# Performance work log

Measured on AMD Instinct MI355X. Metric: run time of the kernel, lower is better.

Reference implementation:

```python
import jax, jax.numpy as jnp
import numpy as np

B = 4096          # batch_size
D_EMB = 16        # per-side embedding dim (embed_to_from width = 2*D_EMB)
D_HIGH = 784      # flattened high-dim feature size
NSR = 5           # negative_sample_rate
A = 1.576943      # UMAP _a
B_PARAM = 0.8950608  # UMAP _b
REPULSION = 1.0
EPS = 1e-4
GLOBAL_LOSS = 0.5
TOTAL_STEPS = 1000
BATCH_COUNT = 500  # fixed step for deterministic alpha/beta
WARMUP = int(0.05 * TOTAL_STEPS)


def _safe_sqrt(sq):
    # sqrt with zero (not NaN) gradient at 0, matching zero-distance pairs
    safe = jnp.where(sq > 0, sq, 1.0)
    return jnp.where(sq > 0, jnp.sqrt(safe), 0.0)


def _pairwise_dist(x):
    # ||x_i - x_j|| via gram trick; avoids materializing [N,N,D]
    sq = jnp.sum(x * x, axis=1)                      # [N]
    gram = x @ x.T                                   # [N,N]
    d2 = sq[:, None] + sq[None, :] - 2.0 * gram
    return _safe_sqrt(jnp.maximum(d2, 0.0))


def _umap_ce_loss(embed_to_from, perm):
    e_to, e_from = jnp.split(embed_to_from, 2, axis=1)   # [B, D_EMB] each
    neg_to = jnp.repeat(e_to, NSR, axis=0)               # [B*NSR, D_EMB]
    repeat_neg = jnp.repeat(e_from, NSR, axis=0)
    neg_from = repeat_neg[perm]                          # shuffled negatives
    d_pos = _safe_sqrt(jnp.sum((e_to - e_from) ** 2, axis=1))
    d_neg = _safe_sqrt(jnp.sum((neg_to - neg_from) ** 2, axis=1))
    dist = jnp.concatenate([d_pos, d_neg], axis=0)       # [B*(1+NSR)]
    p_dist = 1.0 / (1.0 + A * dist ** (2.0 * B_PARAM))
    p_graph = jnp.concatenate([jnp.ones(B, p_dist.dtype), jnp.zeros(B * NSR, p_dist.dtype)])
    attraction = -p_graph * jnp.log(jnp.clip(p_dist, EPS, 1.0))
    repellant = -(1.0 - p_graph) * jnp.log(jnp.clip(1.0 - p_dist, EPS, 1.0)) * REPULSION
    return jnp.mean(attraction + repellant)


def _global_feature_loss(embed_to_from, to_x):
    e_to = embed_to_from[:, :D_EMB]
    to_x = to_x.reshape(to_x.shape[0], -1)
    high_dis = _pairwise_dist(to_x)     # [N,N]
    low_dis = _pairwise_dist(e_to)      # [N,N]
    # row-wise pearson correlation between high_dis and low_dis
    h = high_dis - jnp.mean(high_dis, axis=1, keepdims=True)
    l = low_dis - jnp.mean(low_dis, axis=1, keepdims=True)
    num = jnp.sum(h * l, axis=1)
    den = jnp.sqrt(jnp.sum(h * h, axis=1)) * jnp.sqrt(jnp.sum(l * l, axis=1))
    corr = jnp.mean(num / den)
    return -corr


def _alpha_beta():
    if BATCH_COUNT >= WARMUP:
        if BATCH_COUNT <= 0.9 * TOTAL_STEPS:
            beta = max(0.0, GLOBAL_LOSS * (1 - BATCH_COUNT / (TOTAL_STEPS - WARMUP * 4)) ** 2)
        else:
            beta = 0.0
        alpha = max(0.0, 1 - beta)
    else:
        alpha = 0.0
        beta = GLOBAL_LOSS
    return alpha, beta


def setup_inputs() -> dict:
    key = jax.random.key(0)
    k1, k2, k3 = jax.random.split(key, 3)
    embed_to_from = jax.random.normal(k1, (B, 2 * D_EMB), dtype=jnp.float32)
    placeholder = jax.random.normal(k2, (B, D_HIGH), dtype=jnp.float32)
    perm = jax.random.permutation(k3, B * NSR).astype(jnp.int32)
    return {"embed_to_from": embed_to_from, "placeholder": placeholder, "perm": perm}


def reference(embed_to_from, placeholder, perm):
    loss = _umap_ce_loss(embed_to_from, perm)
    loss_g = _global_feature_loss(embed_to_from, placeholder)
    alpha, beta = _alpha_beta()
    return alpha * loss + beta * loss_g
```

## Files before the change

kernel.cpp:

```cpp
#include <hip/hip_runtime.h>
#include <hip/hip_bf16.h>
#include <math.h>

#define NB    4096
#define DH    784
#define KX8   832
#define NSR   5
#define NNEG  (NB*NSR)
#define NTOT  (NB + NNEG)

#define A_CONST 1.576943f
#define PEXP    1.7901216f
#define EPS_C   1.0e-4f
#define ALPHA_C 0.9296875f
#define BETA_C  0.0703125f

#define NSLOT 64
#define SLAB  (NB * NSLOT)
#define NBLK  528
#define BUFB  8192

typedef __hip_bfloat16 bf16;
typedef short bf16x8 __attribute__((ext_vector_type(8)));
typedef float f32x4  __attribute__((ext_vector_type(4)));

#define WS_XF8    0
#define WS_EBF    3407872
#define WS_SQX    3670016
#define WS_SQE    3686400
#define WS_STATSP 3702784
#define WS_UPART  8945664
#define WS_CPART  8946048
#define WS_CNT    8946304

__device__ __forceinline__ void gl2lds16(const void* g, void* l) {
    __builtin_amdgcn_global_load_lds(
        (const __attribute__((address_space(1))) unsigned int*)g,
        (__attribute__((address_space(3))) unsigned int*)l,
        16, 0, 0);
}

__global__ void prep_fused(const float* __restrict__ X, const float* __restrict__ emb,
                           const int* __restrict__ perm, unsigned char* __restrict__ Xf8,
                           float* __restrict__ sqx, bf16* __restrict__ Ebf,
                           float* __restrict__ sqe, float* __restrict__ upart,
                           unsigned* __restrict__ cnt) {
    if (blockIdx.x == 0 && threadIdx.x == 0) *cnt = 0u;
    if (blockIdx.x < 1024) {
        const int wave = threadIdx.x >> 6, lane = threadIdx.x & 63;
        const int row = blockIdx.x * 4 + wave;
        const float4* xr = (const float4*)(X + (size_t)row * DH);
        int* xb = (int*)(Xf8 + (size_t)row * KX8);
        float s = 0.f;
        #pragma unroll
        for (int it = 0; it < 4; ++it) {
            const int idx = lane + it * 64;
            if (idx < 196) {
                float4 v = xr[idx];
                s += v.x * v.x + v.y * v.y + v.z * v.z + v.w * v.w;
                int lo = __builtin_amdgcn_cvt_pk_fp8_f32(v.x, v.y, 0, false);
                int pk = __builtin_amdgcn_cvt_pk_fp8_f32(v.z, v.w, lo, true);
                xb[idx] = pk;
            } else if (idx < 208) {
                xb[idx] = 0;
            }
        }
        #pragma unroll
        for (int off = 32; off; off >>= 1) s += __shfl_down(s, off, 64);
        if (lane == 0) sqx[row] = s;
        return;
    }
    const int ub = blockIdx.x - 1024;
    const int t = ub * 256 + threadIdx.x;
    float val = 0.f;
    if (t < NB) {
        const float4* av = (const float4*)(emb + (size_t)t * 32);
        float4 t0 = av[0], t1 = av[1], t2 = av[2], t3 = av[3];
        float4 f0 = av[4], f1 = av[5], f2 = av[6], f3 = av[7];
        bf16* eb = Ebf + (size_t)t * 32;
        union { bf16 h[4]; ushort4 u; } cv;
        #define ST4(dst, q) cv.h[0]=__float2bfloat16(q.x); cv.h[1]=__float2bfloat16(q.y); \
                            cv.h[2]=__float2bfloat16(q.z); cv.h[3]=__float2bfloat16(q.w); \
                            *(ushort4*)(dst) = cv.u;
        ST4(eb,      t0) ST4(eb + 4,  t1) ST4(eb + 8,  t2) ST4(eb + 12, t3)
        #undef ST4
        ushort4 z = {0, 0, 0, 0};
        *(ushort4*)(eb + 16) = z; *(ushort4*)(eb + 20) = z;
        *(ushort4*)(eb + 24) = z; *(ushort4*)(eb + 28) = z;
        sqe[t] = t0.x*t0.x + t0.y*t0.y + t0.z*t0.z + t0.w*t0.w
               + t1.x*t1.x + t1.y*t1.y + t1.z*t1.z + t1.w*t1.w
               + t2.x*t2.x + t2.y*t2.y + t2.z*t2.z + t2.w*t2.w
               + t3.x*t3.x + t3.y*t3.y + t3.z*t3.z + t3.w*t3.w;
        float d2 = 0.f;
        #define D2(a, b) { float4 df = {a.x-b.x, a.y-b.y, a.z-b.z, a.w-b.w}; \
                           d2 += df.x*df.x + df.y*df.y + df.z*df.z + df.w*df.w; }
        D2(t0, f0) D2(t1, f1) D2(t2, f2) D2(t3, f3)
        #undef D2
        float d = sqrtf(d2);
        float p = 1.f / (1.f + A_CONST * powf(d, PEXP));
        val = -logf(fminf(fmaxf(p, EPS_C), 1.f));
    } else if (t < NTOT) {
        const int k = t - NB;
        const int ti = k / 5;
        const int fi = perm[k] / 5;
        const float4* at = (const float4*)(emb + (size_t)ti * 32);
        const float4* bt = (const float4*)(emb + (size_t)fi * 32 + 16);
        float d2 = 0.f;
        #pragma unroll
        for (int q = 0; q < 4; ++q) {
            float4 a = at[q], b = bt[q];
            float4 df = {a.x-b.x, a.y-b.y, a.z-b.z, a.w-b.w};
            d2 += df.x*df.x + df.y*df.y + df.z*df.z + df.w*df.w;
        }
        float d = sqrtf(d2);
        float p = 1.f / (1.f + A_CONST * powf(d, PEXP));
        val = -logf(fminf(fmaxf(1.f - p, EPS_C), 1.f));
    }
    #pragma unroll
    for (int off = 32; off; off >>= 1) val += __shfl_down(val, off, 64);
    __shared__ float ps[4];
    if ((threadIdx.x & 63) == 0) ps[threadIdx.x >> 6] = val;
    __syncthreads();
    if (threadIdx.x == 0) upart[ub] = ps[0] + ps[1] + ps[2] + ps[3];
}

__global__ __launch_bounds__(256, 3) void gram_kernel(
    const unsigned char* __restrict__ Xf8, const bf16* __restrict__ Ebf,
    const float* __restrict__ sqx, const float* __restrict__ sqe,
    float* __restrict__ statsp) {
    __shared__ unsigned char As[2 * BUFB];
    __shared__ unsigned char Bs[2 * BUFB];
    __shared__ float sqxs[256];
    __shared__ float sqes[256];

    int n = (blockIdx.x & 7) * 66 + (blockIdx.x >> 3);
    int bi = 0;
    while (n >= 32 - bi) { n -= 32 - bi; ++bi; }
    const int bj = bi + n;
    const int i0 = bi * 128, j0 = bj * 128;

    const int tid  = threadIdx.x;
    const int wave = tid >> 6;
    const int lane = tid & 63;
    const int wy = wave >> 1, wx = wave & 1;
    const int quad = lane >> 4, l15 = lane & 15;

    f32x4 acc[4][4];
    #pragma unroll
    for (int a = 0; a < 4; ++a)
        #pragma unroll
        for (int b = 0; b < 4; ++b)
            acc[a][b] = (f32x4){0.f, 0.f, 0.f, 0.f};

    const int c0  = wave * 2;
    const int rA  = lane >> 2;
    const int gsb = (((lane & 3) ^ ((lane >> 3) & 3))) * 16;

    const unsigned char* gA0 = Xf8 + (size_t)(i0 + c0 * 16 + rA) * KX8 + gsb;
    const unsigned char* gA1 = Xf8 + (size_t)(i0 + c0 * 16 + 16 + rA) * KX8 + gsb;
    const unsigned char* gB0 = Xf8 + (size_t)(j0 + c0 * 16 + rA) * KX8 + gsb;
    const unsigned char* gB1 = Xf8 + (size_t)(j0 + c0 * 16 + 16 + rA) * KX8 + gsb;

    gl2lds16(gA0, As + c0 * 1024);
    gl2lds16(gA1, As + c0 * 1024 + 1024);
    gl2lds16(gB0, Bs + c0 * 1024);
    gl2lds16(gB1, Bs + c0 * 1024 + 1024);
    gA0 += 64; gA1 += 64; gB0 += 64; gB1 += 64;

    if (tid < 128) {
        sqxs[tid] = sqx[i0 + tid]; sqxs[128 + tid] = sqx[j0 + tid];
        sqes[tid] = sqe[i0 + tid]; sqes[128 + tid] = sqe[j0 + tid];
    }

    const int key = (l15 >> 1) & 3;
    const int bo0 = (((quad >> 1) ^ key) << 4)       + (quad & 1) * 8;
    const int bo1 = (((2 + (quad >> 1)) ^ key) << 4) + (quad & 1) * 8;
    const int boE = ((quad ^ key) << 4);

    for (int t = 0; t < 13; ++t) {
        __syncthreads();
        const int cur = (t & 1) * BUFB;
        const int nb  = ((t + 1) & 1) * BUFB;
        if (t < 12) {
            gl2lds16(gA0, As + nb + c0 * 1024);
            gl2lds16(gA1, As + nb + c0 * 1024 + 1024);
            gl2lds16(gB0, Bs + nb + c0 * 1024);
            gl2lds16(gB1, Bs + nb + c0 * 1024 + 1024);
            gA0 += 64; gA1 += 64; gB0 += 64; gB1 += 64;
        } else {
            gl2lds16((const unsigned char*)(Ebf + (size_t)(i0 + c0 * 16 + rA) * 32) + gsb,
                     As + nb + c0 * 1024);
            gl2lds16((const unsigned char*)(Ebf + (size_t)(i0 + c0 * 16 + 16 + rA) * 32) + gsb,
                     As + nb + c0 * 1024 + 1024);
            gl2lds16((const unsigned char*)(Ebf + (size_t)(j0 + c0 * 16 + rA) * 32) + gsb,
                     Bs + nb + c0 * 1024);
            gl2lds16((const unsigned char*)(Ebf + (size_t)(j0 + c0 * 16 + 16 + rA) * 32) + gsb,
                     Bs + nb + c0 * 1024 + 1024);
        }
        long a0[4], a1[4], b0[4], b1[4];
        #pragma unroll
        for (int mi = 0; mi < 4; ++mi) {
            const int r = cur + (wy * 64 + mi * 16 + l15) * 64;
            a0[mi] = *(const long*)&As[r + bo0];
            a1[mi] = *(const long*)&As[r + bo1];
        }
        #pragma unroll
        for (int ni = 0; ni < 4; ++ni) {
            const int r = cur + (wx * 64 + ni * 16 + l15) * 64;
            b0[ni] = *(const long*)&Bs[r + bo0];
            b1[ni] = *(const long*)&Bs[r + bo1];
        }
        #pragma unroll
        for (int mi = 0; mi < 4; ++mi)
            #pragma unroll
            for (int ni = 0; ni < 4; ++ni) {
                acc[mi][ni] = __builtin_amdgcn_mfma_f32_16x16x32_fp8_fp8(
                    a0[mi], b0[ni], acc[mi][ni], 0, 0, 0);
                acc[mi][ni] = __builtin_amdgcn_mfma_f32_16x16x32_fp8_fp8(
                    a1[mi], b1[ni], acc[mi][ni], 0, 0, 0);
            }
    }
    __syncthreads();

    const int slot_r = bj * 2 + wx;
    const int slot_c = bi * 2 + wy;
    bf16x8 bfrE[4];
    #pragma unroll
    for (int ni = 0; ni < 4; ++ni)
        bfrE[ni] = *(const bf16x8*)&Bs[BUFB + (wx * 64 + ni * 16 + l15) * 64 + boE];
    float cH[4] = {0,0,0,0}, cH2[4] = {0,0,0,0}, cL[4] = {0,0,0,0},
          cL2[4] = {0,0,0,0}, cHL[4] = {0,0,0,0};
    #pragma unroll
    for (int mi = 0; mi < 4; ++mi) {
        bf16x8 afE = *(const bf16x8*)&As[BUFB + (wy * 64 + mi * 16 + l15) * 64 + boE];
        f32x4 aE[4];
        #pragma unroll
        for (int ni = 0; ni < 4; ++ni) {
            f32x4 z = (f32x4){0.f, 0.f, 0.f, 0.f};
            aE[ni] = __builtin_amdgcn_mfma_f32_16x16x32_bf16(afE, bfrE[ni], z, 0, 0, 0);
        }
        const int ilocb = wy * 64 + mi * 16 + quad * 4;
        float sH[4] = {0,0,0,0}, sH2[4] = {0,0,0,0}, sL[4] = {0,0,0,0},
              sL2[4] = {0,0,0,0}, sHL[4] = {0,0,0,0};
        #pragma unroll
        for (int ni = 0; ni < 4; ++ni) {
            const int jloc = wx * 64 + ni * 16 + l15;
            const int j = j0 + jloc;
            const float sqxj = sqxs[128 + jloc];
            const float sqej = sqes[128 + jloc];
            #pragma unroll
            for (int r = 0; r < 4; ++r) {
                const int iloc = ilocb + r;
                const int i = i0 + iloc;
                float H, L;
                if (i == j) { H = 0.f; L = 0.f; }
                else {
                    float d2  = sqxs[iloc] + sqxj - 2.0f * acc[mi][ni][r];
                    H = sqrtf(fmaxf(d2, 0.f));
                    float d2e = sqes[iloc] + sqej - 2.0f * aE[ni][r];
                    L = sqrtf(fmaxf(d2e, 0.f));
                }
                sH[r] += H; sH2[r] += H * H; sL[r] += L; sL2[r] += L * L; sHL[r] += H * L;
                cH[ni] += H; cH2[ni] += H * H; cL[ni] += L; cL2[ni] += L * L; cHL[ni] += H * L;
            }
        }
        #pragma unroll
        for (int r = 0; r < 4; ++r) {
            float v0 = sH[r], v1 = sH2[r], v2 = sL[r], v3 = sL2[r], v4 = sHL[r];
            #pragma unroll
            for (int off2 = 1; off2 < 16; off2 <<= 1) {
                v0 += __shfl_xor(v0, off2, 64);
                v1 += __shfl_xor(v1, off2, 64);
                v2 += __shfl_xor(v2, off2, 64);
                v3 += __shfl_xor(v3, off2, 64);
                v4 += __shfl_xor(v4, off2, 64);
            }
            if (l15 == 0) {
                const int i = i0 + ilocb + r;
                float* base = statsp + (size_t)slot_r * NB + i;
                base[0 * SLAB] = v0;
                base[1 * SLAB] = v1;
                base[2 * SLAB] = v2;
                base[3 * SLAB] = v3;
                base[4 * SLAB] = v4;
            }
        }
    }
    if (bi != bj) {
        #pragma unroll
        for (int ni = 0; ni < 4; ++ni) {
            float v0 = cH[ni], v1 = cH2[ni], v2 = cL[ni], v3 = cL2[ni], v4 = cHL[ni];
            #pragma unroll
            for (int off2 = 16; off2 < 64; off2 <<= 1) {
                v0 += __shfl_xor(v0, off2, 64);
                v1 += __shfl_xor(v1, off2, 64);
                v2 += __shfl_xor(v2, off2, 64);
                v3 += __shfl_xor(v3, off2, 64);
                v4 += __shfl_xor(v4, off2, 64);
            }
            if (quad == 0) {
                const int j = j0 + wx * 64 + ni * 16 + l15;
                float* base = statsp + (size_t)slot_c * NB + j;
                base[0 * SLAB] = v0;
                base[1 * SLAB] = v1;
                base[2 * SLAB] = v2;
                base[3 * SLAB] = v3;
                base[4 * SLAB] = v4;
            }
        }
    }
}

__global__ void finish1_kernel(const float* __restrict__ statsp, const float* __restrict__ upart,
                               float* __restrict__ cpart, unsigned* __restrict__ cnt,
                               float* __restrict__ out) {
    __shared__ float ps2[4][64][5];
    const int t = threadIdx.x;
    const int rloc = t & 63;
    const int sg = t >> 6;
    const int r = blockIdx.x * 64 + rloc;
    float sh = 0.f, sh2 = 0.f, sl = 0.f, sl2 = 0.f, shl = 0.f;
    for (int s = sg * 16; s < sg * 16 + 16; ++s) {
        const float* base = statsp + (size_t)s * NB + r;
        sh  += base[0 * SLAB];
        sh2 += base[1 * SLAB];
        sl  += base[2 * SLAB];
        sl2 += base[3 * SLAB];
        shl += base[4 * SLAB];
    }
    ps2[sg][rloc][0] = sh; ps2[sg][rloc][1] = sh2; ps2[sg][rloc][2] = sl;
    ps2[sg][rloc][3] = sl2; ps2[sg][rloc][4] = shl;
    __syncthreads();
    if (t < 64) {
        float a = 0.f, b = 0.f, c = 0.f, d = 0.f, e = 0.f;
        #pragma unroll
        for (int g = 0; g < 4; ++g) {
            a += ps2[g][t][0]; b += ps2[g][t][1]; c += ps2[g][t][2];
            d += ps2[g][t][3]; e += ps2[g][t][4];
        }
        const float invN = 1.0f / (float)NB;
        float num = e - a * c * invN;
        float vh  = fmaxf(b - a * a * invN, 0.f);
        float vl  = fmaxf(d - c * c * invN, 0.f);
        float local = num / (sqrtf(vh) * sqrtf(vl));
        #pragma unroll
        for (int off = 32; off; off >>= 1) local += __shfl_down(local, off, 64);
        if (t == 0) cpart[blockIdx.x] = local;
    }
    __shared__ int lastFlag;
    if (t == 0) {
        __threadfence();
        unsigned prev = atomicAdd(cnt, 1u);
        lastFlag = (prev == 63u);
    }
    __syncthreads();
    if (lastFlag) {
        __threadfence();
        float v = 0.f;
        if (t < 64) v += cpart[t] * (-BETA_C / (float)NB);
        if (t < 96) v += upart[t] * (ALPHA_C / (float)NTOT);
        #pragma unroll
        for (int off = 32; off; off >>= 1) v += __shfl_down(v, off, 64);
        __shared__ float fin[4];
        if ((t & 63) == 0) fin[t >> 6] = v;
        __syncthreads();
        if (t == 0) out[0] = fin[0] + fin[1] + fin[2] + fin[3];
    }
}

extern "C" void kernel_launch(void* const* d_in, const int* in_sizes, int n_in,
                              void* d_out, int out_size, void* d_ws, size_t ws_size,
                              hipStream_t stream) {
    const float* emb  = (const float*)d_in[0];
    const float* ph   = (const float*)d_in[1];
    const int*   perm = (const int*)d_in[2];
    float* out = (float*)d_out;

    char* ws = (char*)d_ws;
    unsigned char* Xf8 = (unsigned char*)(ws + WS_XF8);
    bf16*  Ebf    = (bf16*) (ws + WS_EBF);
    float* sqx    = (float*)(ws + WS_SQX);
    float* sqe    = (float*)(ws + WS_SQE);
    float* statsp = (float*)(ws + WS_STATSP);
    float* upart  = (float*)(ws + WS_UPART);
    float* cpart  = (float*)(ws + WS_CPART);
    unsigned* cnt = (unsigned*)(ws + WS_CNT);

    prep_fused<<<1120, 256, 0, stream>>>(ph, emb, perm, Xf8, sqx, Ebf, sqe, upart, cnt);
    gram_kernel<<<NBLK, 256, 0, stream>>>(Xf8, Ebf, sqx, sqe, statsp);
    finish1_kernel<<<64, 256, 0, stream>>>(statsp, upart, cpart, cnt, out);
}
```

Baseline: 120.2 us.

## Triple-buffer gram K-loop with vmcnt waits and permuted fp8 layout for 16B loads

New measurement: 118.8 us. Within noise of the previous version (-1.2%).

```diff
diff --git a/kernel.cpp b/kernel.cpp
--- a/kernel.cpp
+++ b/kernel.cpp
@@ -23,6 +23,7 @@
 typedef __hip_bfloat16 bf16;
 typedef short bf16x8 __attribute__((ext_vector_type(8)));
 typedef float f32x4  __attribute__((ext_vector_type(4)));
+typedef long long2v __attribute__((ext_vector_type(2)));
 
 #define WS_XF8    0
 #define WS_EBF    3407872
@@ -55,14 +56,18 @@
         #pragma unroll
         for (int it = 0; it < 4; ++it) {
             const int idx = lane + it * 64;
-            if (idx < 196) {
-                float4 v = xr[idx];
-                s += v.x * v.x + v.y * v.y + v.z * v.z + v.w * v.w;
-                int lo = __builtin_amdgcn_cvt_pk_fp8_f32(v.x, v.y, 0, false);
-                int pk = __builtin_amdgcn_cvt_pk_fp8_f32(v.z, v.w, lo, true);
+            if (idx < 208) {
+                const int c = idx >> 4, p = idx & 15;
+                const int q = p >> 2, h = (p >> 1) & 1, w = p & 1;
+                const int src = c * 16 + h * 8 + q * 2 + w;
+                int pk = 0;
+                if (src < 196) {
+                    float4 v = xr[src];
+                    s += v.x * v.x + v.y * v.y + v.z * v.z + v.w * v.w;
+                    int lo = __builtin_amdgcn_cvt_pk_fp8_f32(v.x, v.y, 0, false);
+                    pk = __builtin_amdgcn_cvt_pk_fp8_f32(v.z, v.w, lo, true);
+                }
                 xb[idx] = pk;
-            } else if (idx < 208) {
-                xb[idx] = 0;
             }
         }
         #pragma unroll
@@ -128,8 +133,8 @@
     const unsigned char* __restrict__ Xf8, const bf16* __restrict__ Ebf,
     const float* __restrict__ sqx, const float* __restrict__ sqe,
     float* __restrict__ statsp) {
-    __shared__ unsigned char As[2 * BUFB];
-    __shared__ unsigned char Bs[2 * BUFB];
+    __shared__ unsigned char As[3 * BUFB];
+    __shared__ unsigned char Bs[3 * BUFB];
     __shared__ float sqxs[256];
     __shared__ float sqes[256];
 
@@ -161,78 +166,77 @@
     const unsigned char* gB0 = Xf8 + (size_t)(j0 + c0 * 16 + rA) * KX8 + gsb;
     const unsigned char* gB1 = Xf8 + (size_t)(j0 + c0 * 16 + 16 + rA) * KX8 + gsb;
 
-    gl2lds16(gA0, As + c0 * 1024);
-    gl2lds16(gA1, As + c0 * 1024 + 1024);
-    gl2lds16(gB0, Bs + c0 * 1024);
-    gl2lds16(gB1, Bs + c0 * 1024 + 1024);
-    gA0 += 64; gA1 += 64; gB0 += 64; gB1 += 64;
-
     if (tid < 128) {
         sqxs[tid] = sqx[i0 + tid]; sqxs[128 + tid] = sqx[j0 + tid];
         sqes[tid] = sqe[i0 + tid]; sqes[128 + tid] = sqe[j0 + tid];
     }
+    __syncthreads();
+
+    #pragma unroll
+    for (int s = 0; s < 2; ++s) {
+        gl2lds16(gA0, As + s * BUFB + c0 * 1024);
+        gl2lds16(gA1, As + s * BUFB + c0 * 1024 + 1024);
+        gl2lds16(gB0, Bs + s * BUFB + c0 * 1024);
+        gl2lds16(gB1, Bs + s * BUFB + c0 * 1024 + 1024);
+        gA0 += 64; gA1 += 64; gB0 += 64; gB1 += 64;
+    }
 
     const int key = (l15 >> 1) & 3;
-    const int bo0 = (((quad >> 1) ^ key) << 4)       + (quad & 1) * 8;
-    const int bo1 = (((2 + (quad >> 1)) ^ key) << 4) + (quad & 1) * 8;
-    const int boE = ((quad ^ key) << 4);
-
+    const int boX = ((quad ^ key) << 4);
+
+    int cur = 0;
     for (int t = 0; t < 13; ++t) {
-        __syncthreads();
-        const int cur = (t & 1) * BUFB;
-        const int nb  = ((t + 1) & 1) * BUFB;
-        if (t < 12) {
+        asm volatile("s_waitcnt vmcnt(4)" ::: "memory");
+        __builtin_amdgcn_s_barrier();
+        const int nb = (cur + 2 * BUFB >= 3 * BUFB) ? cur - BUFB : cur + 2 * BUFB;
+        if (t < 11) {
             gl2lds16(gA0, As + nb + c0 * 1024);
             gl2lds16(gA1, As + nb + c0 * 1024 + 1024);
             gl2lds16(gB0, Bs + nb + c0 * 1024);
             gl2lds16(gB1, Bs + nb + c0 * 1024 + 1024);
             gA0 += 64; gA1 += 64; gB0 += 64; gB1 += 64;
-        } else {
+        } else if (t == 11) {
             gl2lds16((const unsigned char*)(Ebf + (size_t)(i0 + c0 * 16 + rA) * 32) + gsb,
-                     As + nb + c0 * 1024);
+                     As + BUFB + c0 * 1024);
             gl2lds16((const unsigned char*)(Ebf + (size_t)(i0 + c0 * 16 + 16 + rA) * 32) + gsb,
-                     As + nb + c0 * 1024 + 1024);
+                     As + BUFB + c0 * 1024 + 1024);
             gl2lds16((const unsigned char*)(Ebf + (size_t)(j0 + c0 * 16 + rA) * 32) + gsb,
-                     Bs + nb + c0 * 1024);
+                     Bs + BUFB + c0 * 1024);
             gl2lds16((const unsigned char*)(Ebf + (size_t)(j0 + c0 * 16 + 16 + rA) * 32) + gsb,
-                     Bs + nb + c0 * 1024 + 1024);
-        }
-        long a0[4], a1[4], b0[4], b1[4];
-        #pragma unroll
-        for (int mi = 0; mi < 4; ++mi) {
-            const int r = cur + (wy * 64 + mi * 16 + l15) * 64;
-            a0[mi] = *(const long*)&As[r + bo0];
-            a1[mi] = *(const long*)&As[r + bo1];
-        }
-        #pragma unroll
-        for (int ni = 0; ni < 4; ++ni) {
-            const int r = cur + (wx * 64 + ni * 16 + l15) * 64;
-            b0[ni] = *(const long*)&Bs[r + bo0];
-            b1[ni] = *(const long*)&Bs[r + bo1];
-        }
+                     Bs + BUFB + c0 * 1024 + 1024);
+        }
+        long2v aF[4], bF[4];
+        #pragma unroll
+        for (int mi = 0; mi < 4; ++mi)
+            aF[mi] = *(const long2v*)&As[cur + (wy * 64 + mi * 16 + l15) * 64 + boX];
+        #pragma unroll
+        for (int ni = 0; ni < 4; ++ni)
+            bF[ni] = *(const long2v*)&Bs[cur + (wx * 64 + ni * 16 + l15) * 64 + boX];
         #pragma unroll
         for (int mi = 0; mi < 4; ++mi)
             #pragma unroll
             for (int ni = 0; ni < 4; ++ni) {
                 acc[mi][ni] = __builtin_amdgcn_mfma_f32_16x16x32_fp8_fp8(
-                    a0[mi], b0[ni], acc[mi][ni], 0, 0, 0);
+                    aF[mi][0], bF[ni][0], acc[mi][ni], 0, 0, 0);
                 acc[mi][ni] = __builtin_amdgcn_mfma_f32_16x16x32_fp8_fp8(
-                    a1[mi], b1[ni], acc[mi][ni], 0, 0, 0);
-            }
-    }
-    __syncthreads();
+                    aF[mi][1], bF[ni][1], acc[mi][ni], 0, 0, 0);
+            }
+        cur = (cur == 2 * BUFB) ? 0 : cur + BUFB;
+    }
+    asm volatile("s_waitcnt vmcnt(0)" ::: "memory");
+    __builtin_amdgcn_s_barrier();
 
     const int slot_r = bj * 2 + wx;
     const int slot_c = bi * 2 + wy;
     bf16x8 bfrE[4];
     #pragma unroll
     for (int ni = 0; ni < 4; ++ni)
-        bfrE[ni] = *(const bf16x8*)&Bs[BUFB + (wx * 64 + ni * 16 + l15) * 64 + boE];
+        bfrE[ni] = *(const bf16x8*)&Bs[BUFB + (wx * 64 + ni * 16 + l15) * 64 + boX];
     float cH[4] = {0,0,0,0}, cH2[4] = {0,0,0,0}, cL[4] = {0,0,0,0},
           cL2[4] = {0,0,0,0}, cHL[4] = {0,0,0,0};
     #pragma unroll
     for (int mi = 0; mi < 4; ++mi) {
-        bf16x8 afE = *(const bf16x8*)&As[BUFB + (wy * 64 + mi * 16 + l15) * 64 + boE];
+        bf16x8 afE = *(const bf16x8*)&As[BUFB + (wy * 64 + mi * 16 + l15) * 64 + boX];
         f32x4 aE[4];
         #pragma unroll
         for (int ni = 0; ni < 4; ++ni) {
```
